# Kernel optimization log

Hardware: AMD Instinct MI355X
Metric: run time of the kernel (lower is better)

## Reference

```python
import jax, jax.numpy as jnp
import numpy as np

EPS = 1e-4

def setup_inputs() -> dict:
    key = jax.random.key(0)
    k1, k2, k3 = jax.random.split(key, 3)
    batch, keysize, dict_size, categories = 4096, 512, 16384, 100
    x = jax.random.normal(k1, (batch, keysize), dtype=jnp.float32)
    keys = jax.random.normal(k2, (dict_size, keysize), dtype=jnp.float32) * 0.1  # TruncatedNormal(0, 0.1) approx
    values = jax.random.uniform(k3, (dict_size, categories), dtype=jnp.float32)
    return {"x": x, "keys": keys, "values": values}


def reference(x, keys, values):
    # sq_distance(keys, x): (dict_size, batch)
    kk = jnp.sum(keys * keys, axis=1)[:, None]          # (D, 1)
    xx = jnp.sum(x * x, axis=1)[None, :]                # (1, B)
    d = kk - 2.0 * jnp.matmul(keys, x.T) + xx           # (D, B)
    kern = 1.0 / (d + EPS)                              # reciprocal kernel
    # transpose -> (B, D), matmul values (D, C) -> (B, C)
    return jnp.matmul(kern.T, values)
```

## Files before the change

### kernel.cpp

```cpp
#include <hip/hip_runtime.h>
#include <hip/hip_bf16.h>
#include <hip/hip_fp8.h>
#include <cstdint>


#define BSZ   4096
#define DSZ   16384
#define KSZ   512
#define CC    100
#define CP    128
#define EPSV  1e-4f

#define BM     64
#define BD     64
#define DSPLIT 8
#define DCHUNK (DSZ / DSPLIT)
#define NITER  (DCHUNK / BD)
#define KTS    72

typedef short  short8 __attribute__((ext_vector_type(8)));
typedef float  f32x4  __attribute__((ext_vector_type(4)));
typedef long   lng2   __attribute__((ext_vector_type(2)));
typedef unsigned int   u32;
typedef unsigned short u16;
typedef unsigned char  u8;

__device__ __forceinline__ u16 f2bf(float f) {
    union { float f; u32 u; } cv; cv.f = f;
    u32 u = cv.u;
    u += 0x7fffu + ((u >> 16) & 1u);
    return (u16)(u >> 16);
}
__device__ __forceinline__ u32 pack2(float a, float b) {
    return (u32)f2bf(a) | ((u32)f2bf(b) << 16);
}
__device__ __forceinline__ u8 f2fp8(float f) {
    __hip_fp8_e4m3 t(f);
    return *reinterpret_cast<u8*>(&t);
}

__device__ __forceinline__ void gload_lds16(const void* g, void* l) {
    __builtin_amdgcn_global_load_lds(
        (const __attribute__((address_space(1))) u32*)g,
        (__attribute__((address_space(3))) u32*)l, 16, 0, 0);
}


__global__ __launch_bounds__(256)
void convert_xk(const float* __restrict__ x, const float* __restrict__ keys,
                u8* __restrict__ xw, u8* __restrict__ kw,
                float* __restrict__ kk, float* __restrict__ xx)
{
    const int tid = threadIdx.x, wid = tid >> 6, lane = tid & 63;
    const int row = blockIdx.x * 4 + wid;
    const float* src; u8* dst; float* nrm; int r;
    if (row < DSZ) { r = row;       src = keys + (size_t)r * KSZ; dst = kw + (size_t)r * KSZ; nrm = kk + r; }
    else           { r = row - DSZ; src = x    + (size_t)r * KSZ; dst = xw + (size_t)r * KSZ; nrm = xx + r; }

    float4 v0 = *reinterpret_cast<const float4*>(src + lane * 8);
    float4 v1 = *reinterpret_cast<const float4*>(src + lane * 8 + 4);
    float s = v0.x*v0.x + v0.y*v0.y + v0.z*v0.z + v0.w*v0.w
            + v1.x*v1.x + v1.y*v1.y + v1.z*v1.z + v1.w*v1.w;

    unsigned long long pk = 0;
    pk |= (unsigned long long)f2fp8(v0.x);
    pk |= (unsigned long long)f2fp8(v0.y) << 8;
    pk |= (unsigned long long)f2fp8(v0.z) << 16;
    pk |= (unsigned long long)f2fp8(v0.w) << 24;
    pk |= (unsigned long long)f2fp8(v1.x) << 32;
    pk |= (unsigned long long)f2fp8(v1.y) << 40;
    pk |= (unsigned long long)f2fp8(v1.z) << 48;
    pk |= (unsigned long long)f2fp8(v1.w) << 56;

    const int j = lane >> 2, hi_l = lane & 3;
    const int ch = j >> 3, jl = j & 7, jj = jl >> 1, f = jl & 1;
    const int off = ch * 256 + (((jj * 64 + hi_l * 16)) ^ ((r & 7) << 4)) + f * 8;
    *reinterpret_cast<unsigned long long*>(dst + off) = pk;

    s += __shfl_xor(s, 1);  s += __shfl_xor(s, 2);  s += __shfl_xor(s, 4);
    s += __shfl_xor(s, 8);  s += __shfl_xor(s, 16); s += __shfl_xor(s, 32);
    if (lane == 0) *nrm = s;
}

__global__ __launch_bounds__(256)
void convert_v(const float* __restrict__ values, u16* __restrict__ vw)
{
    const int gid = blockIdx.x * 256 + threadIdx.x;
    const int c = gid >> 11;
    const int j = gid & 2047;
    const int dp  = ((j >> 3) << 6) + ((j & 7) << 3);
    const int dsg = ((j >> 3) << 6) + (((j & 7) ^ (c & 7)) << 3);
    uint4 w = make_uint4(0, 0, 0, 0);
    if (c < CC) {
        float f[8];
#pragma unroll
        for (int i = 0; i < 8; ++i) f[i] = values[(size_t)(dsg + i) * CC + c];
        w.x = pack2(f[0], f[1]); w.y = pack2(f[2], f[3]);
        w.z = pack2(f[4], f[5]); w.w = pack2(f[6], f[7]);
    }
    *reinterpret_cast<uint4*>(vw + (size_t)c * DSZ + dp) = w;
}

__global__ __launch_bounds__(512, 4)
void varkeys_fast(const u8* __restrict__ xw, const u8* __restrict__ kw,
                  const u16* __restrict__ vw, const float* __restrict__ kkp,
                  const float* __restrict__ xxp, float* __restrict__ out)
{
    __shared__ __align__(16) u8  ksb0[BD * 256];
    __shared__ __align__(16) u8  ksb1[BD * 256];
    __shared__ __align__(16) u16 kT[BM * KTS];
    __shared__ __align__(16) u16 vT[CP * BD];
    __shared__ float xx_s[BM];

    const int tid  = threadIdx.x;
    const int wid  = tid >> 6;
    const int lane = tid & 63;
    const int lo   = lane & 15;
    const int hi   = lane >> 4;
    const int wm   = wid >> 1;
    const int wn   = wid & 1;

    const int h  = blockIdx.x;
    const int by = h & 7, bx = h >> 3;
    const int bm0   = bx * BM;
    const int dbase = by * DCHUNK;

    if (tid < BM) xx_s[tid] = xxp[bm0 + tid];

    lng2 xq[8];
    {
        const int row = bm0 + wm * 16 + lo;
        const u8* base = xw + (size_t)row * KSZ;
        const int s16 = (row & 7) << 4;
#pragma unroll
        for (int ch = 0; ch < 2; ++ch)
#pragma unroll
            for (int jj = 0; jj < 4; ++jj)
                xq[ch * 4 + jj] = *reinterpret_cast<const lng2*>(
                    base + ch * 256 + ((jj * 64 + hi * 16) ^ s16));
    }

    f32x4 accO[4];
#pragma unroll
    for (int n = 0; n < 4; ++n) accO[n] = f32x4{0.f, 0.f, 0.f, 0.f};

#define IS_KS(BUFP, DK, CCH) { \
        _Pragma("unroll") \
        for (int i = 0; i < 2; ++i) { \
            const int ci = wid * 2 + i; \
            const int flat = ci * 1024 + lane * 16; \
            gload_lds16(kw + (size_t)((DK) + (flat >> 8)) * KSZ + (CCH) * 256 + (flat & 255), \
                        (char*)(BUFP) + ci * 1024); \
        } }

#define IS_VT(D0) { \
        _Pragma("unroll") \
        for (int i = 0; i < 2; ++i) { \
            const int ci = wid * 2 + i; \
            const int flat = ci * 512 + lane * 8; \
            gload_lds16(vw + (size_t)(flat >> 6) * DSZ + (D0) + (flat & 63), \
                        (char*)vT + ci * 1024); \
        } }

    IS_KS(ksb0, dbase, 0)
    asm volatile("s_waitcnt lgkmcnt(0)" ::: "memory");
    __builtin_amdgcn_s_barrier();

    const int swz   = (lo & 7) << 3;
    const int swz16 = (lo & 7) << 4;

#define A16(CH, BUF)                                                                  \
    {                                                                                 \
        _Pragma("unroll")                                                             \
        for (int jj = 0; jj < 4; ++jj) {                                              \
            const int off = (jj * 64 + hi * 16) ^ swz16;                              \
            const u8* p0 = (const u8*)(BUF) + (wn * 32 + lo) * 256 + off;             \
            lng2 b0 = *reinterpret_cast<const lng2*>(p0);                             \
            lng2 b1 = *reinterpret_cast<const lng2*>(p0 + 16 * 256);                  \
            lng2 a0 = xq[(CH) * 4 + jj];                                              \
            accS[0] = __builtin_amdgcn_mfma_f32_16x16x32_fp8_fp8(a0[0], b0[0], accS[0], 0, 0, 0); \
            accS[1] = __builtin_amdgcn_mfma_f32_16x16x32_fp8_fp8(a0[0], b1[0], accS[1], 0, 0, 0); \
            accS[0] = __builtin_amdgcn_mfma_f32_16x16x32_fp8_fp8(a0[1], b0[1], accS[0], 0, 0, 0); \
            accS[1] = __builtin_amdgcn_mfma_f32_16x16x32_fp8_fp8(a0[1], b1[1], accS[1], 0, 0, 0); \
        }                                                                             \
    }

    for (int it = 0; it < NITER; ++it) {
        const int d0 = dbase + it * BD;

        f32x4 accS[2];
#pragma unroll
        for (int n = 0; n < 2; ++n) accS[n] = f32x4{0.f, 0.f, 0.f, 0.f};

        __builtin_amdgcn_s_barrier();
        IS_KS(ksb1, d0, 1)
        IS_VT(d0)
        const float kkf0 = kkp[d0 + wn * 32 + lo];
        const float kkf1 = kkp[d0 + wn * 32 + 16 + lo];
        asm volatile("s_waitcnt vmcnt(6)" ::: "memory");
        __builtin_amdgcn_s_barrier();
        __builtin_amdgcn_sched_barrier(0);
        A16(0, ksb0)

        __builtin_amdgcn_s_barrier();
        if (it < NITER - 1) {
            IS_KS(ksb0, d0 + BD, 0)
            asm volatile("s_waitcnt vmcnt(6)" ::: "memory");
        } else {
            asm volatile("s_waitcnt vmcnt(0)" ::: "memory");
        }
        __builtin_amdgcn_s_barrier();
        __builtin_amdgcn_sched_barrier(0);
        A16(1, ksb1)

#pragma unroll
        for (int n = 0; n < 2; ++n) {
            const int dl = wn * 32 + n * 16 + lo;
            const float kkv = n ? kkf1 : kkf0;
#pragma unroll
            for (int r = 0; r < 4; ++r) {
                const int rowl = wm * 16 + hi * 4 + r;
                const float dsq = kkv + xx_s[rowl] - 2.f * accS[n][r] + EPSV;
                kT[rowl * KTS + dl] = f2bf(__builtin_amdgcn_rcpf(dsq));
            }
        }
        asm volatile("s_waitcnt vmcnt(2)" ::: "memory");
        asm volatile("s_waitcnt lgkmcnt(0)" ::: "memory");
        __builtin_amdgcn_s_barrier();
        __builtin_amdgcn_sched_barrier(0);

#pragma unroll
        for (int kst = 0; kst < 2; ++kst) {
            const int k0l = kst * 32 + hi * 8;
            const int k0v = k0l ^ swz;
            short8 a0 = *reinterpret_cast<const short8*>(&kT[(wm * 16 + lo) * KTS + k0l]);
#pragma unroll
            for (int nh = 0; nh < 2; ++nh) {
                short8 b0 = *reinterpret_cast<const short8*>(&vT[(wn * 64 + nh * 32 + lo) * BD + k0v]);
                short8 b1 = *reinterpret_cast<const short8*>(&vT[(wn * 64 + nh * 32 + 16 + lo) * BD + k0v]);
                accO[nh * 2 + 0] = __builtin_amdgcn_mfma_f32_16x16x32_bf16(a0, b0, accO[nh * 2 + 0], 0, 0, 0);
                accO[nh * 2 + 1] = __builtin_amdgcn_mfma_f32_16x16x32_bf16(a0, b1, accO[nh * 2 + 1], 0, 0, 0);
            }
        }
    }

#pragma unroll
    for (int n = 0; n < 4; ++n) {
        const int c = wn * 64 + n * 16 + lo;
        if (c < CC) {
#pragma unroll
            for (int r = 0; r < 4; ++r) {
                const int b_ = bm0 + wm * 16 + hi * 4 + r;
                atomicAdd(&out[(size_t)b_ * CC + c], accO[n][r]);
            }
        }
    }
#undef IS_KS
#undef IS_VT
#undef A16
}


#define FBM 128
#define XS_STRIDE 72
#define KS_STRIDE 72
#define KT_STRIDE 72
#define VL_STRIDE 106
#define FKC 64
#define FNKC (KSZ / FKC)
#define FDSPLIT 8
#define FDCHUNK (DSZ / FDSPLIT)
#define FNITER  (FDCHUNK / BD)

__global__ __launch_bounds__(256)
void varkeys_pre(const float* __restrict__ x, const float* __restrict__ keys,
                 float* __restrict__ kk, float* __restrict__ xx)
{
    const int tid  = threadIdx.x;
    const int wid  = tid >> 6;
    const int lane = tid & 63;
    const int lo   = lane & 15;
    const int sub  = lane >> 4;
    const int row  = blockIdx.x * 16 + wid * 4 + sub;
    const float* src = (row < DSZ) ? keys + (size_t)row * KSZ
                                   : x + (size_t)(row - DSZ) * KSZ;
    float s = 0.f;
#pragma unroll
    for (int j = 0; j < 8; ++j) {
        float4 v = *reinterpret_cast<const float4*>(src + j * 64 + lo * 4);
        s += v.x * v.x + v.y * v.y + v.z * v.z + v.w * v.w;
    }
    s += __shfl_xor(s, 1); s += __shfl_xor(s, 2);
    s += __shfl_xor(s, 4); s += __shfl_xor(s, 8);
    if (lo == 0) {
        if (row < DSZ) kk[row] = s;
        else           xx[row - DSZ] = s;
    }
}

__global__ __launch_bounds__(256, 2)
void varkeys_main(const float* __restrict__ x, const float* __restrict__ keys,
                  const float* __restrict__ values, float* __restrict__ out,
                  const float* __restrict__ kk_ws, const float* __restrict__ xx_ws,
                  int use_ws)
{
    __shared__ __align__(16) u16 xs[FBM * XS_STRIDE];
    __shared__ __align__(16) u16 ks[BD * KS_STRIDE];
    __shared__ __align__(16) u16 kTf[FBM * KT_STRIDE];
    __shared__ __align__(16) u16 vls[BD * VL_STRIDE];
    __shared__ float kk_s[FDCHUNK];
    __shared__ float xx_s[FBM];

    const int tid  = threadIdx.x;
    const int wid  = tid >> 6;
    const int lane = tid & 63;
    const int lo   = lane & 15;
    const int hi   = lane >> 4;
    const int wm   = wid >> 1;
    const int wn   = wid & 1;
    const int bm0   = blockIdx.x * FBM;
    const int dbase = blockIdx.y * FDCHUNK;

    if (use_ws) {
        for (int i = tid; i < FDCHUNK; i += 256) kk_s[i] = kk_ws[dbase + i];
        if (tid < FBM) xx_s[tid] = xx_ws[bm0 + tid];
    } else {
        for (int rbase = wid * 4; rbase < FDCHUNK + FBM; rbase += 16) {
            const int row = rbase + hi;
            const float* src = (row < FDCHUNK)
                ? keys + (size_t)(dbase + row) * KSZ
                : x + (size_t)(bm0 + row - FDCHUNK) * KSZ;
            float s = 0.f;
#pragma unroll
            for (int j = 0; j < 8; ++j) {
                float4 v = *reinterpret_cast<const float4*>(src + j * 64 + lo * 4);
                s += v.x * v.x + v.y * v.y + v.z * v.z + v.w * v.w;
            }
            s += __shfl_xor(s, 1); s += __shfl_xor(s, 2);
            s += __shfl_xor(s, 4); s += __shfl_xor(s, 8);
            if (lo == 0) {
                if (row < FDCHUNK) kk_s[row] = s;
                else               xx_s[row - FDCHUNK] = s;
            }
        }
    }
    __syncthreads();

    f32x4 accO[4][4];
#pragma unroll
    for (int m = 0; m < 4; ++m)
#pragma unroll
        for (int n = 0; n < 4; ++n) accO[m][n] = f32x4{0.f, 0.f, 0.f, 0.f};

    for (int it = 0; it < FNITER; ++it) {
        const int d0 = dbase + it * BD;

        f32x4 accS[4][2];
#pragma unroll
        for (int m = 0; m < 4; ++m)
#pragma unroll
            for (int n = 0; n < 2; ++n) accS[m][n] = f32x4{0.f, 0.f, 0.f, 0.f};

        for (int kc = 0; kc < FNKC; ++kc) {
            __syncthreads();
#pragma unroll
            for (int j = 0; j < 8; ++j) {
                const int idx = tid + j * 256;
                const int row = idx >> 4, c4 = idx & 15;
                float4 v = *reinterpret_cast<const float4*>(
                    x + (size_t)(bm0 + row) * KSZ + kc * FKC + c4 * 4);
                u32* dst = reinterpret_cast<u32*>(&xs[row * XS_STRIDE + c4 * 4]);
                dst[0] = pack2(v.x, v.y); dst[1] = pack2(v.z, v.w);
            }
#pragma unroll
            for (int j = 0; j < 4; ++j) {
                const int idx = tid + j * 256;
                const int row = idx >> 4, c4 = idx & 15;
                float4 v = *reinterpret_cast<const float4*>(
                    keys + (size_t)(d0 + row) * KSZ + kc * FKC + c4 * 4);
                u32* dst = reinterpret_cast<u32*>(&ks[row * KS_STRIDE + c4 * 4]);
                dst[0] = pack2(v.x, v.y); dst[1] = pack2(v.z, v.w);
            }
            __syncthreads();
#pragma unroll
            for (int kst = 0; kst < 2; ++kst) {
                const int k0 = kst * 32 + hi * 8;
                short8 a[4], b[2];
#pragma unroll
                for (int m = 0; m < 4; ++m)
                    a[m] = *reinterpret_cast<const short8*>(
                        &xs[(wm * 64 + m * 16 + lo) * XS_STRIDE + k0]);
#pragma unroll
                for (int n = 0; n < 2; ++n)
                    b[n] = *reinterpret_cast<const short8*>(
                        &ks[(wn * 32 + n * 16 + lo) * KS_STRIDE + k0]);
#pragma unroll
                for (int m = 0; m < 4; ++m)
#pragma unroll
                    for (int n = 0; n < 2; ++n)
                        accS[m][n] = __builtin_amdgcn_mfma_f32_16x16x32_bf16(
                            a[m], b[n], accS[m][n], 0, 0, 0);
            }
        }

#pragma unroll
        for (int m = 0; m < 4; ++m)
#pragma unroll
            for (int n = 0; n < 2; ++n) {
                const int dl = wn * 32 + n * 16 + lo;
                const float kkv = kk_s[it * BD + dl];
#pragma unroll
                for (int r = 0; r < 4; ++r) {
                    const int bl = wm * 64 + m * 16 + hi * 4 + r;
                    const float dsq = kkv + xx_s[bl] - 2.f * accS[m][n][r] + EPSV;
                    kTf[bl * KT_STRIDE + dl] = f2bf(__builtin_amdgcn_rcpf(dsq));
                }
            }

#pragma unroll
        for (int j = 0; j < 7; ++j) {
            const int idx = tid + j * 256;
            if (idx < 1600) {
                const int row = idx / 25, c4 = idx % 25;
                float4 v = *reinterpret_cast<const float4*>(
                    values + (size_t)(d0 + row) * CC + c4 * 4);
                u32* dst = reinterpret_cast<u32*>(&vls[row * VL_STRIDE + c4 * 4]);
                dst[0] = pack2(v.x, v.y); dst[1] = pack2(v.z, v.w);
            }
        }
        __syncthreads();

#pragma unroll
        for (int ks2 = 0; ks2 < 2; ++ks2) {
            const int k0 = ks2 * 32 + hi * 8;
            short8 a[4], b[4];
#pragma unroll
            for (int m = 0; m < 4; ++m)
                a[m] = *reinterpret_cast<const short8*>(
                    &kTf[(wm * 64 + m * 16 + lo) * KT_STRIDE + k0]);
#pragma unroll
            for (int n = 0; n < 4; ++n) {
                const int c = wn * 64 + n * 16 + lo;
                short8 t = {0, 0, 0, 0, 0, 0, 0, 0};
                if (c < CC) {
#pragma unroll
                    for (int i = 0; i < 8; ++i)
                        t[i] = (short)vls[(k0 + i) * VL_STRIDE + c];
                }
                b[n] = t;
            }
#pragma unroll
            for (int m = 0; m < 4; ++m)
#pragma unroll
                for (int n = 0; n < 4; ++n)
                    accO[m][n] = __builtin_amdgcn_mfma_f32_16x16x32_bf16(
                        a[m], b[n], accO[m][n], 0, 0, 0);
        }
    }

#pragma unroll
    for (int m = 0; m < 4; ++m)
#pragma unroll
        for (int n = 0; n < 4; ++n) {
            const int c = wn * 64 + n * 16 + lo;
            if (c < CC) {
#pragma unroll
                for (int r = 0; r < 4; ++r) {
                    const int b_ = bm0 + wm * 64 + m * 16 + hi * 4 + r;
                    atomicAdd(&out[(size_t)b_ * CC + c], accO[m][n][r]);
                }
            }
        }
}

extern "C" void kernel_launch(void* const* d_in, const int* in_sizes, int n_in,
                              void* d_out, int out_size, void* d_ws, size_t ws_size,
                              hipStream_t stream) {
    const float* x      = (const float*)d_in[0];
    const float* keys   = (const float*)d_in[1];
    const float* values = (const float*)d_in[2];
    float* out = (float*)d_out;

    hipMemsetAsync(d_out, 0, (size_t)out_size * sizeof(float), stream);

    const size_t off_xw = 0;
    const size_t off_kw = off_xw + (size_t)BSZ * KSZ;
    const size_t off_vw = off_kw + (size_t)DSZ * KSZ;
    const size_t off_kk = off_vw + (size_t)CP * DSZ * 2;
    const size_t off_xx = off_kk + (size_t)DSZ * 4;
    const size_t need   = off_xx + (size_t)BSZ * 4;

    if (ws_size >= need) {
        u8*  xw = (u8*)((char*)d_ws + off_xw);
        u8*  kw = (u8*)((char*)d_ws + off_kw);
        u16* vw = (u16*)((char*)d_ws + off_vw);
        float* kk = (float*)((char*)d_ws + off_kk);
        float* xx = (float*)((char*)d_ws + off_xx);
        convert_xk<<<dim3((DSZ + BSZ) / 4), dim3(256), 0, stream>>>(x, keys, xw, kw, kk, xx);
        convert_v<<<dim3((CP * DSZ / 8) / 256), dim3(256), 0, stream>>>(values, vw);
        varkeys_fast<<<dim3(DSPLIT * (BSZ / BM)), dim3(512), 0, stream>>>(xw, kw, vw, kk, xx, out);
    } else {
        const size_t ws_need = (size_t)(DSZ + BSZ) * sizeof(float);
        const int use_ws = (ws_size >= ws_need) ? 1 : 0;
        float* kk = (float*)d_ws;
        float* xx = kk + DSZ;
        if (use_ws) {
            varkeys_pre<<<dim3((DSZ + BSZ) / 16), dim3(256), 0, stream>>>(x, keys, kk, xx);
        }
        varkeys_main<<<dim3(BSZ / FBM, FDSPLIT), dim3(256), 0, stream>>>(
            x, keys, values, out, kk, xx, use_ws);
    }
}
```

Baseline: 114.6 us.

## Pre-swizzle fp8 keys into MFMA fragment layout and load them directly from global

The key conversion kernel now writes fp8 keys in a layout where each 1 KB block holds exactly one MFMA B-fragment for a 16-row group, so each lane reads 16 contiguous bytes. The main kernel drops the double-buffered LDS staging of keys and its barriers, loading key fragments straight from global/L2 into registers before the fp8 MFMAs. This frees LDS and removes sync points, but exposes global load latency on the critical path without software prefetch, and the two wn-waves in a block each fetch their own keys from L2 rather than sharing staged data.

```diff
diff --git a/kernel.cpp b/kernel.cpp
--- a/kernel.cpp
+++ b/kernel.cpp
@@ -48,14 +48,14 @@
 
 __global__ __launch_bounds__(256)
 void convert_xk(const float* __restrict__ x, const float* __restrict__ keys,
-                u8* __restrict__ xw, u8* __restrict__ kw,
+                u8* __restrict__ xw, u8* __restrict__ kw2,
                 float* __restrict__ kk, float* __restrict__ xx)
 {
     const int tid = threadIdx.x, wid = tid >> 6, lane = tid & 63;
     const int row = blockIdx.x * 4 + wid;
-    const float* src; u8* dst; float* nrm; int r;
-    if (row < DSZ) { r = row;       src = keys + (size_t)r * KSZ; dst = kw + (size_t)r * KSZ; nrm = kk + r; }
-    else           { r = row - DSZ; src = x    + (size_t)r * KSZ; dst = xw + (size_t)r * KSZ; nrm = xx + r; }
+    const bool is_k = (row < DSZ);
+    const int r = is_k ? row : row - DSZ;
+    const float* src = is_k ? keys + (size_t)r * KSZ : x + (size_t)r * KSZ;
 
     float4 v0 = *reinterpret_cast<const float4*>(src + lane * 8);
     float4 v1 = *reinterpret_cast<const float4*>(src + lane * 8 + 4);
@@ -72,14 +72,22 @@
     pk |= (unsigned long long)f2fp8(v1.z) << 48;
     pk |= (unsigned long long)f2fp8(v1.w) << 56;
 
-    const int j = lane >> 2, hi_l = lane & 3;
-    const int ch = j >> 3, jl = j & 7, jj = jl >> 1, f = jl & 1;
-    const int off = ch * 256 + (((jj * 64 + hi_l * 16)) ^ ((r & 7) << 4)) + f * 8;
-    *reinterpret_cast<unsigned long long*>(dst + off) = pk;
+    if (is_k) {
+        const int jp = lane >> 2;
+        const int ch = jp >> 3, jj = (jp & 7) >> 1, f = jp & 1;
+        const int lane_t = (lane & 3) * 16 + (r & 15);
+        const size_t addr = ((size_t)((r >> 4) * 8 + ch * 4 + jj) << 10) + lane_t * 16 + f * 8;
+        *reinterpret_cast<unsigned long long*>(kw2 + addr) = pk;
+    } else {
+        const int j = lane >> 2, hi_l = lane & 3;
+        const int ch = j >> 3, jl = j & 7, jj = jl >> 1, f = jl & 1;
+        const int off = ch * 256 + (((jj * 64 + hi_l * 16)) ^ ((r & 7) << 4)) + f * 8;
+        *reinterpret_cast<unsigned long long*>(xw + (size_t)r * KSZ + off) = pk;
+    }
 
     s += __shfl_xor(s, 1);  s += __shfl_xor(s, 2);  s += __shfl_xor(s, 4);
     s += __shfl_xor(s, 8);  s += __shfl_xor(s, 16); s += __shfl_xor(s, 32);
-    if (lane == 0) *nrm = s;
+    if (lane == 0) { if (is_k) kk[r] = s; else xx[r] = s; }
 }
 
 __global__ __launch_bounds__(256)
@@ -102,12 +110,10 @@
 }
 
 __global__ __launch_bounds__(512, 4)
-void varkeys_fast(const u8* __restrict__ xw, const u8* __restrict__ kw,
+void varkeys_fast(const u8* __restrict__ xw, const u8* __restrict__ kw2,
                   const u16* __restrict__ vw, const float* __restrict__ kkp,
                   const float* __restrict__ xxp, float* __restrict__ out)
 {
-    __shared__ __align__(16) u8  ksb0[BD * 256];
-    __shared__ __align__(16) u8  ksb1[BD * 256];
     __shared__ __align__(16) u16 kT[BM * KTS];
     __shared__ __align__(16) u16 vT[CP * BD];
     __shared__ float xx_s[BM];
@@ -143,15 +149,6 @@
     f32x4 accO[4];
 #pragma unroll
     for (int n = 0; n < 4; ++n) accO[n] = f32x4{0.f, 0.f, 0.f, 0.f};
-
-#define IS_KS(BUFP, DK, CCH) { \
-        _Pragma("unroll") \
-        for (int i = 0; i < 2; ++i) { \
-            const int ci = wid * 2 + i; \
-            const int flat = ci * 1024 + lane * 16; \
-            gload_lds16(kw + (size_t)((DK) + (flat >> 8)) * KSZ + (CCH) * 256 + (flat & 255), \
-                        (char*)(BUFP) + ci * 1024); \
-        } }
 
 #define IS_VT(D0) { \
         _Pragma("unroll") \
@@ -162,56 +159,42 @@
                         (char*)vT + ci * 1024); \
         } }
 
-    IS_KS(ksb0, dbase, 0)
     asm volatile("s_waitcnt lgkmcnt(0)" ::: "memory");
     __builtin_amdgcn_s_barrier();
 
-    const int swz   = (lo & 7) << 3;
-    const int swz16 = (lo & 7) << 4;
-
-#define A16(CH, BUF)                                                                  \
-    {                                                                                 \
-        _Pragma("unroll")                                                             \
-        for (int jj = 0; jj < 4; ++jj) {                                              \
-            const int off = (jj * 64 + hi * 16) ^ swz16;                              \
-            const u8* p0 = (const u8*)(BUF) + (wn * 32 + lo) * 256 + off;             \
-            lng2 b0 = *reinterpret_cast<const lng2*>(p0);                             \
-            lng2 b1 = *reinterpret_cast<const lng2*>(p0 + 16 * 256);                  \
-            lng2 a0 = xq[(CH) * 4 + jj];                                              \
-            accS[0] = __builtin_amdgcn_mfma_f32_16x16x32_fp8_fp8(a0[0], b0[0], accS[0], 0, 0, 0); \
-            accS[1] = __builtin_amdgcn_mfma_f32_16x16x32_fp8_fp8(a0[0], b1[0], accS[1], 0, 0, 0); \
-            accS[0] = __builtin_amdgcn_mfma_f32_16x16x32_fp8_fp8(a0[1], b0[1], accS[0], 0, 0, 0); \
-            accS[1] = __builtin_amdgcn_mfma_f32_16x16x32_fp8_fp8(a0[1], b1[1], accS[1], 0, 0, 0); \
-        }                                                                             \
-    }
+    const int swz = (lo & 7) << 3;
+
+#define ACH(CH) { \
+        lng2 bq0[4], bq1[4]; \
+        _Pragma("unroll") \
+        for (int jj = 0; jj < 4; ++jj) { \
+            bq0[jj] = *reinterpret_cast<const lng2*>( \
+                kw2 + ((size_t)((gb0)     * 8 + (CH) * 4 + jj) << 10) + lane * 16); \
+            bq1[jj] = *reinterpret_cast<const lng2*>( \
+                kw2 + ((size_t)((gb0 + 1) * 8 + (CH) * 4 + jj) << 10) + lane * 16); \
+        } \
+        _Pragma("unroll") \
+        for (int jj = 0; jj < 4; ++jj) { \
+            accS[0] = __builtin_amdgcn_mfma_f32_16x16x32_fp8_fp8(xq[(CH) * 4 + jj][0], bq0[jj][0], accS[0], 0, 0, 0); \
+            accS[1] = __builtin_amdgcn_mfma_f32_16x16x32_fp8_fp8(xq[(CH) * 4 + jj][0], bq1[jj][0], accS[1], 0, 0, 0); \
+            accS[0] = __builtin_amdgcn_mfma_f32_16x16x32_fp8_fp8(xq[(CH) * 4 + jj][1], bq0[jj][1], accS[0], 0, 0, 0); \
+            accS[1] = __builtin_amdgcn_mfma_f32_16x16x32_fp8_fp8(xq[(CH) * 4 + jj][1], bq1[jj][1], accS[1], 0, 0, 0); \
+        } }
 
     for (int it = 0; it < NITER; ++it) {
         const int d0 = dbase + it * BD;
+        const int gb0 = (d0 >> 4) + wn * 2;
 
         f32x4 accS[2];
-#pragma unroll
-        for (int n = 0; n < 2; ++n) accS[n] = f32x4{0.f, 0.f, 0.f, 0.f};
-
-        __builtin_amdgcn_s_barrier();
-        IS_KS(ksb1, d0, 1)
+        accS[0] = f32x4{0.f, 0.f, 0.f, 0.f};
+        accS[1] = f32x4{0.f, 0.f, 0.f, 0.f};
+
         IS_VT(d0)
         const float kkf0 = kkp[d0 + wn * 32 + lo];
         const float kkf1 = kkp[d0 + wn * 32 + 16 + lo];
-        asm volatile("s_waitcnt vmcnt(6)" ::: "memory");
-        __builtin_amdgcn_s_barrier();
-        __builtin_amdgcn_sched_barrier(0);
-        A16(0, ksb0)
-
-        __builtin_amdgcn_s_barrier();
-        if (it < NITER - 1) {
-            IS_KS(ksb0, d0 + BD, 0)
-            asm volatile("s_waitcnt vmcnt(6)" ::: "memory");
-        } else {
-            asm volatile("s_waitcnt vmcnt(0)" ::: "memory");
-        }
-        __builtin_amdgcn_s_barrier();
-        __builtin_amdgcn_sched_barrier(0);
-        A16(1, ksb1)
+
+        ACH(0)
+        ACH(1)
 
 #pragma unroll
         for (int n = 0; n < 2; ++n) {
@@ -224,7 +207,7 @@
                 kT[rowl * KTS + dl] = f2bf(__builtin_amdgcn_rcpf(dsq));
             }
         }
-        asm volatile("s_waitcnt vmcnt(2)" ::: "memory");
+        asm volatile("s_waitcnt vmcnt(0)" ::: "memory");
         asm volatile("s_waitcnt lgkmcnt(0)" ::: "memory");
         __builtin_amdgcn_s_barrier();
         __builtin_amdgcn_sched_barrier(0);
@@ -242,6 +225,9 @@
                 accO[nh * 2 + 1] = __builtin_amdgcn_mfma_f32_16x16x32_bf16(a0, b1, accO[nh * 2 + 1], 0, 0, 0);
             }
         }
+
+        __builtin_amdgcn_s_barrier();
+        __builtin_amdgcn_sched_barrier(0);
     }
 
 #pragma unroll
@@ -255,9 +241,8 @@
             }
         }
     }
-#undef IS_KS
 #undef IS_VT
-#undef A16
+#undef ACH
 }
 
 
@@ -491,14 +476,14 @@
     const size_t need   = off_xx + (size_t)BSZ * 4;
 
     if (ws_size >= need) {
-        u8*  xw = (u8*)((char*)d_ws + off_xw);
-        u8*  kw = (u8*)((char*)d_ws + off_kw);
-        u16* vw = (u16*)((char*)d_ws + off_vw);
+        u8*  xw  = (u8*)((char*)d_ws + off_xw);
+        u8*  kw2 = (u8*)((char*)d_ws + off_kw);
+        u16* vw  = (u16*)((char*)d_ws + off_vw);
         float* kk = (float*)((char*)d_ws + off_kk);
         float* xx = (float*)((char*)d_ws + off_xx);
-        convert_xk<<<dim3((DSZ + BSZ) / 4), dim3(256), 0, stream>>>(x, keys, xw, kw, kk, xx);
+        convert_xk<<<dim3((DSZ + BSZ) / 4), dim3(256), 0, stream>>>(x, keys, xw, kw2, kk, xx);
         convert_v<<<dim3((CP * DSZ / 8) / 256), dim3(256), 0, stream>>>(values, vw);
-        varkeys_fast<<<dim3(DSPLIT * (BSZ / BM)), dim3(512), 0, stream>>>(xw, kw, vw, kk, xx, out);
+        varkeys_fast<<<dim3(DSPLIT * (BSZ / BM)), dim3(512), 0, stream>>>(xw, kw2, vw, kk, xx, out);
     } else {
         const size_t ws_need = (size_t)(DSZ + BSZ) * sizeof(float);
         const int use_ws = (ws_size >= ws_need) ? 1 : 0;
```

New measurement: 147.9 us. +29.0%, slower.
